# Optimization experiments

Hardware: AMD Instinct MI355X
Metric: run time of the kernel (lower is better)

## Reference

```python
import jax, jax.numpy as jnp
import numpy as np

N_NODES = 100000
N_EDGES = 1600000
F_IN, HIDDEN, N_CLASS = 256, 64, 2


def _gcn_conv(x, W, b, src, dst, norm, n):
    # PyG GCNConv: linear (no bias) -> normalized scatter-add -> bias
    h = x @ W                                  # [N, out]
    msg = h[src] * norm[:, None]               # gather + scale, [E+N, out]
    agg = jax.ops.segment_sum(msg, dst, num_segments=n)
    return agg + b


def setup_inputs() -> dict:
    key = jax.random.key(0)
    ks = jax.random.split(key, 8)
    x = jax.random.normal(ks[0], (N_NODES, F_IN), dtype=jnp.float32)
    edge_index = jax.random.randint(ks[1], (2, N_EDGES), 0, N_NODES, dtype=jnp.int32)
    W1 = jax.random.normal(ks[2], (F_IN, HIDDEN), dtype=jnp.float32) / np.sqrt(F_IN).astype(np.float32)
    b1 = jnp.zeros((HIDDEN,), dtype=jnp.float32)
    W2 = jax.random.normal(ks[3], (HIDDEN, HIDDEN), dtype=jnp.float32) / np.sqrt(HIDDEN).astype(np.float32)
    b2 = jnp.zeros((HIDDEN,), dtype=jnp.float32)
    W3 = jax.random.normal(ks[4], (HIDDEN, N_CLASS), dtype=jnp.float32) / np.sqrt(HIDDEN).astype(np.float32)
    b3 = jnp.zeros((N_CLASS,), dtype=jnp.float32)
    return {"x": x, "edge_index": edge_index, "W1": W1, "b1": b1, "W2": W2, "b2": b2, "W3": W3, "b3": b3}


def reference(x, edge_index, W1, b1, W2, b2, W3, b3):
    n = x.shape[0]
    # add self-loops (GCNConv default)
    loops = jnp.arange(n, dtype=edge_index.dtype)
    src = jnp.concatenate([edge_index[0], loops])
    dst = jnp.concatenate([edge_index[1], loops])
    # symmetric normalization D^-1/2 A_hat D^-1/2
    deg = jax.ops.segment_sum(jnp.ones_like(src, dtype=x.dtype), dst, num_segments=n)
    deg_inv_sqrt = jnp.where(deg > 0, jax.lax.rsqrt(jnp.maximum(deg, 1.0)), 0.0)
    norm = deg_inv_sqrt[src] * deg_inv_sqrt[dst]
    # layer 1 + relu (dropout is identity in eval mode)
    h = jax.nn.relu(_gcn_conv(x, W1, b1, src, dst, norm, n))
    # layer 2 + relu
    h = jax.nn.relu(_gcn_conv(h, W2, b2, src, dst, norm, n))
    # output layer + log_softmax
    h = _gcn_conv(h, W3, b3, src, dst, norm, n)
    return jax.nn.log_softmax(h, axis=1)
```

## Files before the change

kernel.cpp:

```cpp
#include <hip/hip_runtime.h>
#include <math.h>

#define F_IN 256
#define HID  64
#define BSH  8
#define BSPAN 256
#define CHUNK 16384
#define NBK_MAX 512

typedef __bf16   bf16x8 __attribute__((ext_vector_type(8)));
typedef float    floatx4 __attribute__((ext_vector_type(4)));
typedef _Float16 half8 __attribute__((ext_vector_type(8)));

__global__ __launch_bounds__(256) void k_hist(const int* __restrict__ dst,
                                              int* __restrict__ cntT,
                                              int E, int NCH, int NBK) {
    __shared__ int hist[NBK_MAX];
    int t = threadIdx.x, c = blockIdx.x;
    hist[t] = 0; hist[t + 256] = 0;
    __syncthreads();
    int base = c * CHUNK;
#pragma unroll 4
    for (int j = 0; j < CHUNK / 256; j++) {
        int e = base + j * 256 + t;
        if (e < E) atomicAdd(&hist[dst[e] >> BSH], 1);
    }
    __syncthreads();
    for (int b = t; b < NBK; b += 256) cntT[b * NCH + c] = hist[b];
}

__global__ __launch_bounds__(256) void k_scanA(const int* __restrict__ cntT,
                                               int* __restrict__ off,
                                               int* __restrict__ partials, int S) {
    __shared__ int sh[256];
    int tid = threadIdx.x;
    int base = blockIdx.x * 1024 + tid * 4;
    int v[4];
    int s = 0;
#pragma unroll
    for (int j = 0; j < 4; j++) {
        int idx = base + j;
        v[j] = (idx < S) ? cntT[idx] : 0;
        s += v[j];
    }
    sh[tid] = s;
    __syncthreads();
    int mysum = s;
    for (int o = 1; o < 256; o <<= 1) {
        int tv = (tid >= o) ? sh[tid - o] : 0;
        __syncthreads();
        sh[tid] += tv;
        __syncthreads();
    }
    int pref = sh[tid] - mysum;
#pragma unroll
    for (int j = 0; j < 4; j++) {
        int idx = base + j;
        if (idx < S) off[idx] = pref;
        pref += v[j];
    }
    if (tid == 255) partials[blockIdx.x] = sh[255];
}

__global__ void k_scanB(int* __restrict__ partials, int* __restrict__ off,
                        int nblk, int S) {
    if (blockIdx.x == 0 && threadIdx.x == 0) {
        int run = 0;
        for (int b = 0; b < nblk; b++) { int t = partials[b]; partials[b] = run; run += t; }
        off[S] = run;
    }
}

__global__ void k_scanC(int* __restrict__ off, const int* __restrict__ partials, int S) {
    int i = blockIdx.x * blockDim.x + threadIdx.x;
    if (i < S) off[i] += partials[i >> 10];
}

__global__ __launch_bounds__(256) void k_sortwrite(const int* __restrict__ src,
                                                   const int* __restrict__ dst,
                                                   const int* __restrict__ off,
                                                   int* __restrict__ ebuf,
                                                   int E, int NCH, int NBK) {
    __shared__ int cur[NBK_MAX];
    int t = threadIdx.x, c = blockIdx.x;
    for (int b = t; b < NBK; b += 256) cur[b] = off[b * NCH + c];
    __syncthreads();
    int base = c * CHUNK;
#pragma unroll 4
    for (int j = 0; j < CHUNK / 256; j++) {
        int e = base + j * 256 + t;
        if (e < E) {
            int s = src[e];
            int d = dst[e];
            int pos = atomicAdd(&cur[d >> BSH], 1);
            ebuf[pos] = (s << BSH) | (d & (BSPAN - 1));
        }
    }
}

__global__ __launch_bounds__(256) void k_bucket_csr(const int* __restrict__ off,
                                                    const int* __restrict__ ebuf,
                                                    int* __restrict__ rp,
                                                    float* __restrict__ dinv,
                                                    int* __restrict__ esrc,
                                                    int N, int NCH, int NBK) {
    __shared__ int cnt[BSPAN];
    __shared__ int sh[BSPAN];
    int b = blockIdx.x, t = threadIdx.x;
    int base = off[b * NCH];
    int end  = off[(b + 1) * NCH];

    cnt[t] = 0;
    __syncthreads();
    for (int i = base + t; i < end; i += 256) atomicAdd(&cnt[ebuf[i] & (BSPAN - 1)], 1);
    __syncthreads();

    int c = cnt[t];
    sh[t] = c;
    __syncthreads();
    for (int o = 1; o < 256; o <<= 1) {
        int tv = (t >= o) ? sh[t - o] : 0;
        __syncthreads();
        sh[t] += tv;
        __syncthreads();
    }
    int excl = sh[t] - c;

    int node = (b << BSH) + t;
    if (node < N) {
        rp[node] = base + excl;
        dinv[node] = rsqrtf((float)(1 + c));
    }
    if (b == NBK - 1 && t == 0) rp[N] = end;
    __syncthreads();

    cnt[t] = base + excl;
    __syncthreads();
    for (int i = base + t; i < end; i += 256) {
        int v = ebuf[i];
        int p = atomicAdd(&cnt[v & (BSPAN - 1)], 1);
        esrc[p] = v >> BSH;
    }
}

__global__ __launch_bounds__(256) void k_prepw(const float* __restrict__ W1,
                                               __bf16* __restrict__ f1h, __bf16* __restrict__ f1l,
                                               const float* __restrict__ W2,
                                               __bf16* __restrict__ f2h, __bf16* __restrict__ f2l) {
    int t = threadIdx.x + blockIdx.x * blockDim.x;
    for (int idx = t; idx < 16384; idx += 2048) {
        int j = idx & 7, lane = (idx >> 3) & 63, ch2 = (idx >> 9) & 7, c = idx >> 12;
        int k = ch2 * 32 + (lane >> 4) * 8 + j, col = c * 16 + (lane & 15);
        float w = W1[k * 64 + col];
        __bf16 h = (__bf16)w;
        f1h[idx] = h; f1l[idx] = (__bf16)(w - (float)h);
    }
    for (int idx = t; idx < 4096; idx += 2048) {
        int j = idx & 7, lane = (idx >> 3) & 63, ch2 = (idx >> 9) & 1, c = idx >> 10;
        int k = ch2 * 32 + (lane >> 4) * 8 + j, col = c * 16 + (lane & 15);
        float w = W2[k * 64 + col];
        __bf16 h = (__bf16)w;
        f2h[idx] = h; f2l[idx] = (__bf16)(w - (float)h);
    }
}

__global__ __launch_bounds__(256) void k_gemm1(const float* __restrict__ A,
                                               const __bf16* __restrict__ BfH,
                                               const __bf16* __restrict__ BfL,
                                               const float* __restrict__ dinv,
                                               _Float16* __restrict__ C, int nrows) {
    constexpr int K = 256, KC = 64, NCHK = 4, NCH32 = 8;
    __shared__ float As[2][64 * KC];

    const int t = threadIdx.x;
    const int wave = t >> 6, lane = t & 63;
    const int m = lane & 15, q = lane >> 4;
    const int row0 = blockIdx.x * 64;

    const int s_sub = lane >> 4;
    const int s_seg = lane & 15;

    auto stage = [&](int ch, int buf) {
#pragma unroll
        for (int j = 0; j < 4; j++) {
            int lr = wave * 16 + j * 4 + s_sub;
            int gr = row0 + lr; if (gr > nrows - 1) gr = nrows - 1;
            int gs = (s_seg - lr) & 15;
            const float* g = A + (size_t)gr * K + ch * KC + gs * 4;
            float* l = &As[buf][(size_t)lr * KC + s_seg * 4];
            __builtin_amdgcn_global_load_lds(
                (const __attribute__((address_space(1))) void*)g,
                (__attribute__((address_space(3))) void*)l, 16, 0, 0);
        }
    };

    floatx4 acc[4] = {{0.f, 0.f, 0.f, 0.f}, {0.f, 0.f, 0.f, 0.f},
                      {0.f, 0.f, 0.f, 0.f}, {0.f, 0.f, 0.f, 0.f}};

    stage(0, 0);
    __syncthreads();

    for (int ch = 0; ch < NCHK; ch++) {
        if (ch + 1 < NCHK) stage(ch + 1, (ch + 1) & 1);

        const float* arow = &As[ch & 1][(size_t)(wave * 16 + m) * KC];
#pragma unroll
        for (int jj = 0; jj < 2; jj++) {
            int ch2 = ch * 2 + jj;
            int s0 = jj * 8 + q * 2;
            float4 v0 = *(const float4*)(arow + (((s0 + m) & 15) * 4));
            float4 v1 = *(const float4*)(arow + (((s0 + 1 + m) & 15) * 4));
            float af[8] = {v0.x, v0.y, v0.z, v0.w, v1.x, v1.y, v1.z, v1.w};
            bf16x8 ah, al;
#pragma unroll
            for (int j = 0; j < 8; j++) {
                __bf16 h = (__bf16)af[j];
                ah[j] = h;
                al[j] = (__bf16)(af[j] - (float)h);
            }
#pragma unroll
            for (int c = 0; c < 4; c++) {
                const bf16x8 bh = *(const bf16x8*)(BfH + ((size_t)(c * NCH32 + ch2) * 64 + lane) * 8);
                const bf16x8 bl = *(const bf16x8*)(BfL + ((size_t)(c * NCH32 + ch2) * 64 + lane) * 8);
                acc[c] = __builtin_amdgcn_mfma_f32_16x16x32_bf16(ah, bh, acc[c], 0, 0, 0);
                acc[c] = __builtin_amdgcn_mfma_f32_16x16x32_bf16(al, bh, acc[c], 0, 0, 0);
                acc[c] = __builtin_amdgcn_mfma_f32_16x16x32_bf16(ah, bl, acc[c], 0, 0, 0);
            }
        }
        __syncthreads();
    }

#pragma unroll
    for (int i = 0; i < 4; i++) {
        int r = row0 + wave * 16 + q * 4 + i;
        if (r < nrows) {
            float di = dinv[r];
#pragma unroll
            for (int c = 0; c < 4; c++)
                C[(size_t)r * 64 + c * 16 + m] = (_Float16)(acc[c][i] * di);
        }
    }
}

__global__ __launch_bounds__(256) void k_gemm2(const _Float16* __restrict__ A,
                                               const __bf16* __restrict__ BfH,
                                               const __bf16* __restrict__ BfL,
                                               const float* __restrict__ dinv,
                                               _Float16* __restrict__ C, int nrows) {
    __shared__ _Float16 As[64 * 64];
    const int t = threadIdx.x;
    const int wave = t >> 6, lane = t & 63;
    const int m = lane & 15, q = lane >> 4;
    const int row0 = blockIdx.x * 64;

#pragma unroll
    for (int j = 0; j < 2; j++) {
        int lr = j * 32 + wave * 8 + (lane >> 3);
        int p  = lane & 7;
        int gr = row0 + lr; if (gr > nrows - 1) gr = nrows - 1;
        int gs = (p - lr) & 7;
        const _Float16* g = A + (size_t)gr * 64 + gs * 8;
        _Float16* l = &As[(size_t)lr * 64 + p * 8];
        __builtin_amdgcn_global_load_lds(
            (const __attribute__((address_space(1))) void*)g,
            (__attribute__((address_space(3))) void*)l, 16, 0, 0);
    }
    __syncthreads();

    floatx4 acc[4] = {{0.f, 0.f, 0.f, 0.f}, {0.f, 0.f, 0.f, 0.f},
                      {0.f, 0.f, 0.f, 0.f}, {0.f, 0.f, 0.f, 0.f}};

    const _Float16* arow = &As[(size_t)(wave * 16 + m) * 64];
#pragma unroll
    for (int jj = 0; jj < 2; jj++) {
        int s0 = jj * 4 + q;
        half8 v = *(const half8*)(arow + (((s0 + m) & 7) * 8));
        bf16x8 ah, al;
#pragma unroll
        for (int j = 0; j < 8; j++) {
            float f = (float)v[j];
            __bf16 h = (__bf16)f;
            ah[j] = h;
            al[j] = (__bf16)(f - (float)h);
        }
#pragma unroll
        for (int c = 0; c < 4; c++) {
            const bf16x8 bh = *(const bf16x8*)(BfH + ((size_t)(c * 2 + jj) * 64 + lane) * 8);
            const bf16x8 bl = *(const bf16x8*)(BfL + ((size_t)(c * 2 + jj) * 64 + lane) * 8);
            acc[c] = __builtin_amdgcn_mfma_f32_16x16x32_bf16(ah, bh, acc[c], 0, 0, 0);
            acc[c] = __builtin_amdgcn_mfma_f32_16x16x32_bf16(al, bh, acc[c], 0, 0, 0);
            acc[c] = __builtin_amdgcn_mfma_f32_16x16x32_bf16(ah, bl, acc[c], 0, 0, 0);
        }
    }

#pragma unroll
    for (int i = 0; i < 4; i++) {
        int r = row0 + wave * 16 + q * 4 + i;
        if (r < nrows) {
            float di = dinv[r];
#pragma unroll
            for (int c = 0; c < 4; c++)
                C[(size_t)r * 64 + c * 16 + m] = (_Float16)(acc[c][i] * di);
        }
    }
}

template <int MODE>
__global__ __launch_bounds__(256) void k_agg64(const _Float16* __restrict__ hs,
                                               const float* __restrict__ dinv,
                                               const int* __restrict__ rp,
                                               const int* __restrict__ esrc,
                                               const float* __restrict__ bias,
                                               const float* __restrict__ W3,
                                               void* __restrict__ out, int n) {
    int lane = threadIdx.x & 63;
    int nid = blockIdx.x * 4 + (threadIdx.x >> 6);
    if (nid >= n) return;
    nid = __builtin_amdgcn_readfirstlane(nid);

    float dii = dinv[nid];
    int e0 = rp[nid];
    int e1 = rp[nid + 1];

    float a0 = (float)hs[(size_t)nid * 64 + lane];
    float a1 = 0.f, a2 = 0.f, a3 = 0.f, a4 = 0.f, a5 = 0.f, a6 = 0.f, a7 = 0.f;

    for (int e = e0; e < e1; e += 8) {
        int last = e1 - 1;
        int i0 = esrc[e];
        int i1 = esrc[min(e + 1, last)];
        int i2 = esrc[min(e + 2, last)];
        int i3 = esrc[min(e + 3, last)];
        int i4 = esrc[min(e + 4, last)];
        int i5 = esrc[min(e + 5, last)];
        int i6 = esrc[min(e + 6, last)];
        int i7 = esrc[min(e + 7, last)];
        float v0 = (float)hs[(size_t)i0 * 64 + lane];
        float v1 = (float)hs[(size_t)i1 * 64 + lane];
        float v2 = (float)hs[(size_t)i2 * 64 + lane];
        float v3 = (float)hs[(size_t)i3 * 64 + lane];
        float v4 = (float)hs[(size_t)i4 * 64 + lane];
        float v5 = (float)hs[(size_t)i5 * 64 + lane];
        float v6 = (float)hs[(size_t)i6 * 64 + lane];
        float v7 = (float)hs[(size_t)i7 * 64 + lane];
        a0 += v0;
        a1 += (e + 1 <= last) ? v1 : 0.f;
        a2 += (e + 2 <= last) ? v2 : 0.f;
        a3 += (e + 3 <= last) ? v3 : 0.f;
        a4 += (e + 4 <= last) ? v4 : 0.f;
        a5 += (e + 5 <= last) ? v5 : 0.f;
        a6 += (e + 6 <= last) ? v6 : 0.f;
        a7 += (e + 7 <= last) ? v7 : 0.f;
    }

    float acc = ((a0 + a1) + (a2 + a3)) + ((a4 + a5) + (a6 + a7));
    acc = acc * dii + bias[lane];
    acc = fmaxf(acc, 0.f);

    if (MODE == 0) {
        ((_Float16*)out)[(size_t)nid * 64 + lane] = (_Float16)acc;
    } else {
        float2 w3 = ((const float2*)W3)[lane];
        float p0 = acc * w3.x;
        float p1 = acc * w3.y;
#pragma unroll
        for (int o = 32; o > 0; o >>= 1) {
            p0 += __shfl_xor(p0, o, 64);
            p1 += __shfl_xor(p1, o, 64);
        }
        if (lane == 0) ((float2*)out)[nid] = make_float2(p0 * dii, p1 * dii);
    }
}

__global__ __launch_bounds__(256) void k_final(const float2* __restrict__ h3s,
                                               const float* __restrict__ dinv,
                                               const int* __restrict__ rp,
                                               const int* __restrict__ esrc,
                                               const float* __restrict__ b3,
                                               float* __restrict__ out, int n) {
    int i = blockIdx.x * blockDim.x + threadIdx.x;
    if (i >= n) return;
    float dii = dinv[i];
    float2 h = h3s[i];
    float ax = h.x, ay = h.y;
    float bx = 0.f, by = 0.f, cx = 0.f, cy = 0.f, dx = 0.f, dy = 0.f;
    int e0 = rp[i], e1 = rp[i + 1];
    for (int e = e0; e < e1; e += 4) {
        int last = e1 - 1;
        int s0 = esrc[e];
        int s1 = esrc[min(e + 1, last)];
        int s2 = esrc[min(e + 2, last)];
        int s3 = esrc[min(e + 3, last)];
        float2 v0 = h3s[s0];
        float2 v1 = h3s[s1];
        float2 v2 = h3s[s2];
        float2 v3 = h3s[s3];
        ax += v0.x; ay += v0.y;
        bx += (e + 1 <= last) ? v1.x : 0.f; by += (e + 1 <= last) ? v1.y : 0.f;
        cx += (e + 2 <= last) ? v2.x : 0.f; cy += (e + 2 <= last) ? v2.y : 0.f;
        dx += (e + 3 <= last) ? v3.x : 0.f; dy += (e + 3 <= last) ? v3.y : 0.f;
    }
    float l0 = ((ax + bx) + (cx + dx)) * dii + b3[0];
    float l1 = ((ay + by) + (cy + dy)) * dii + b3[1];
    float m = fmaxf(l0, l1);
    float lse = m + logf(expf(l0 - m) + expf(l1 - m));
    ((float2*)out)[i] = make_float2(l0 - lse, l1 - lse);
}

extern "C" void kernel_launch(void* const* d_in, const int* in_sizes, int n_in,
                              void* d_out, int out_size, void* d_ws, size_t ws_size,
                              hipStream_t stream) {
    const float* x   = (const float*)d_in[0];
    const int*   ei  = (const int*)d_in[1];
    const float* W1  = (const float*)d_in[2];
    const float* b1  = (const float*)d_in[3];
    const float* W2  = (const float*)d_in[4];
    const float* b2  = (const float*)d_in[5];
    const float* W3  = (const float*)d_in[6];
    const float* b3  = (const float*)d_in[7];
    float* out = (float*)d_out;

    const int N = in_sizes[0] / F_IN;
    const int E = in_sizes[1] / 2;
    const int* src = ei;
    const int* dst = ei + E;

    const int NBK = (N + BSPAN - 1) / BSPAN;
    const int NCH = (E + CHUNK - 1) / CHUNK;
    const int S   = NBK * NCH;

    char* p = (char*)d_ws;
    auto alloc = [&](size_t bytes) -> void* {
        void* r = (void*)p;
        p += (bytes + 255) & ~(size_t)255;
        return r;
    };
    int*      cntT     = (int*)alloc((size_t)S * 4);
    int*      off      = (int*)alloc((size_t)(S + 1) * 4);
    int*      partials = (int*)alloc(4096);
    int*      ebuf     = (int*)alloc((size_t)E * 4);
    int*      esrc     = (int*)alloc((size_t)E * 4);
    int*      rp       = (int*)alloc((size_t)(N + 1) * 4);
    float*    dinv     = (float*)alloc((size_t)N * 4);
    _Float16* bufA     = (_Float16*)alloc((size_t)N * HID * 2);
    _Float16* bufB     = (_Float16*)alloc((size_t)N * HID * 2);
    float*    h3       = (float*)alloc((size_t)N * 2 * 4);
    __bf16*   f1h      = (__bf16*)alloc(16384 * 2);
    __bf16*   f1l      = (__bf16*)alloc(16384 * 2);
    __bf16*   f2h      = (__bf16*)alloc(4096 * 2);
    __bf16*   f2l      = (__bf16*)alloc(4096 * 2);

    const int T = 256;
    int scanBlocks = (S + 1023) / 1024;

    k_prepw<<<8, T, 0, stream>>>(W1, f1h, f1l, W2, f2h, f2l);

    k_hist<<<NCH, T, 0, stream>>>(dst, cntT, E, NCH, NBK);
    k_scanA<<<scanBlocks, T, 0, stream>>>(cntT, off, partials, S);
    k_scanB<<<1, 64, 0, stream>>>(partials, off, scanBlocks, S);
    k_scanC<<<(S + T - 1) / T, T, 0, stream>>>(off, partials, S);
    k_sortwrite<<<NCH, T, 0, stream>>>(src, dst, off, ebuf, E, NCH, NBK);
    k_bucket_csr<<<NBK, T, 0, stream>>>(off, ebuf, rp, dinv, esrc, N, NCH, NBK);

    int gemmBlocks = (N + 63) / 64;
    k_gemm1<<<gemmBlocks, T, 0, stream>>>(x, f1h, f1l, dinv, bufA, N);
    k_agg64<0><<<(N + 3) / 4, T, 0, stream>>>(bufA, dinv, rp, esrc, b1, nullptr, bufB, N);

    k_gemm2<<<gemmBlocks, T, 0, stream>>>(bufB, f2h, f2l, dinv, bufA, N);
    k_agg64<1><<<(N + 3) / 4, T, 0, stream>>>(bufA, dinv, rp, esrc, b2, W3, h3, N);

    k_final<<<(N + T - 1) / T, T, 0, stream>>>((const float2*)h3, dinv, rp, esrc, b3, out, N);
}
```

Measured before the change: 404.4 us.

## Fuse layer-1 aggregation with layer-2 GEMM, widen gathers, wave-per-node final

Merges the first-layer neighbor aggregation and the second-layer GEMM into one kernel. Each block aggregates 64 nodes into fp32 shared memory with a swizzled layout, then runs the split-bf16 MFMA on that tile. This drops the fp16 round trip through global memory and one launch. The gather loops are unrolled to 16 independent loads for more memory-level parallelism. The final 2-class aggregation now uses one wave per node with lanes over edges and a shuffle reduction. The risks are lower occupancy in the fused kernel, because each wave handles 16 nodes serially with 16 accumulators, and an underused wave in the final kernel, since nodes average about 17 edges.

```diff
diff --git a/kernel.cpp b/kernel.cpp
--- a/kernel.cpp
+++ b/kernel.cpp
@@ -242,77 +242,95 @@
     }
 }
 
-__global__ __launch_bounds__(256) void k_gemm2(const _Float16* __restrict__ A,
-                                               const __bf16* __restrict__ BfH,
-                                               const __bf16* __restrict__ BfL,
-                                               const float* __restrict__ dinv,
-                                               _Float16* __restrict__ C, int nrows) {
-    __shared__ _Float16 As[64 * 64];
+__global__ __launch_bounds__(256) void k_aggemm(const _Float16* __restrict__ hs,
+                                                const float* __restrict__ dinv,
+                                                const int* __restrict__ rp,
+                                                const int* __restrict__ esrc,
+                                                const float* __restrict__ bias,
+                                                const __bf16* __restrict__ BfH,
+                                                const __bf16* __restrict__ BfL,
+                                                _Float16* __restrict__ C, int n) {
+    __shared__ float As[64 * 64];
     const int t = threadIdx.x;
     const int wave = t >> 6, lane = t & 63;
     const int m = lane & 15, q = lane >> 4;
-    const int row0 = blockIdx.x * 64;
-
-#pragma unroll
-    for (int j = 0; j < 2; j++) {
-        int lr = j * 32 + wave * 8 + (lane >> 3);
-        int p  = lane & 7;
-        int gr = row0 + lr; if (gr > nrows - 1) gr = nrows - 1;
-        int gs = (p - lr) & 7;
-        const _Float16* g = A + (size_t)gr * 64 + gs * 8;
-        _Float16* l = &As[(size_t)lr * 64 + p * 8];
-        __builtin_amdgcn_global_load_lds(
-            (const __attribute__((address_space(1))) void*)g,
-            (__attribute__((address_space(3))) void*)l, 16, 0, 0);
-    }
-    __syncthreads();
-
-    floatx4 acc[4] = {{0.f, 0.f, 0.f, 0.f}, {0.f, 0.f, 0.f, 0.f},
-                      {0.f, 0.f, 0.f, 0.f}, {0.f, 0.f, 0.f, 0.f}};
-
-    const _Float16* arow = &As[(size_t)(wave * 16 + m) * 64];
+    const int n0 = blockIdx.x * 64;
+    const int seg = lane >> 2, off = lane & 3;
+    const float bl = bias[lane];
+
+    for (int i = 0; i < 16; i++) {
+        int lr = wave * 16 + i;
+        int nid = n0 + lr;
+        int nn = min(nid, n - 1);
+        float dii = dinv[nn];
+        int e0 = rp[nn], e1 = rp[nn + 1];
+
+        float a[16];
+        a[0] = (float)hs[(size_t)nn * 64 + lane];
+#pragma unroll
+        for (int k2 = 1; k2 < 16; k2++) a[k2] = 0.f;
+
+        for (int e = e0; e < e1; e += 16) {
+            int last = e1 - 1;
+#pragma unroll
+            for (int k2 = 0; k2 < 16; k2++) {
+                int idx = esrc[min(e + k2, last)];
+                float v = (float)hs[(size_t)idx * 64 + lane];
+                a[k2] += (e + k2 <= last) ? v : 0.f;
+            }
+        }
+        float s = (((a[0] + a[1]) + (a[2] + a[3])) + ((a[4] + a[5]) + (a[6] + a[7])))
+                + (((a[8] + a[9]) + (a[10] + a[11])) + ((a[12] + a[13]) + (a[14] + a[15])));
+        float acc = fmaxf(s * dii + bl, 0.f);
+        As[lr * 64 + (((seg + lr) & 15) << 2) + off] = (nid < n) ? acc : 0.f;
+    }
+    __syncthreads();
+
+    floatx4 acc4[4] = {{0.f, 0.f, 0.f, 0.f}, {0.f, 0.f, 0.f, 0.f},
+                       {0.f, 0.f, 0.f, 0.f}, {0.f, 0.f, 0.f, 0.f}};
+    const float* arow = &As[(size_t)(wave * 16 + m) * 64];
 #pragma unroll
     for (int jj = 0; jj < 2; jj++) {
-        int s0 = jj * 4 + q;
-        half8 v = *(const half8*)(arow + (((s0 + m) & 7) * 8));
+        int s0 = jj * 8 + q * 2;
+        float4 v0 = *(const float4*)(arow + (((s0 + m) & 15) * 4));
+        float4 v1 = *(const float4*)(arow + (((s0 + 1 + m) & 15) * 4));
+        float af[8] = {v0.x, v0.y, v0.z, v0.w, v1.x, v1.y, v1.z, v1.w};
         bf16x8 ah, al;
 #pragma unroll
         for (int j = 0; j < 8; j++) {
-            float f = (float)v[j];
-            __bf16 h = (__bf16)f;
+            __bf16 h = (__bf16)af[j];
             ah[j] = h;
-            al[j] = (__bf16)(f - (float)h);
+            al[j] = (__bf16)(af[j] - (float)h);
         }
 #pragma unroll
         for (int c = 0; c < 4; c++) {
             const bf16x8 bh = *(const bf16x8*)(BfH + ((size_t)(c * 2 + jj) * 64 + lane) * 8);
-            const bf16x8 bl = *(const bf16x8*)(BfL + ((size_t)(c * 2 + jj) * 64 + lane) * 8);
-            acc[c] = __builtin_amdgcn_mfma_f32_16x16x32_bf16(ah, bh, acc[c], 0, 0, 0);
-            acc[c] = __builtin_amdgcn_mfma_f32_16x16x32_bf16(al, bh, acc[c], 0, 0, 0);
-            acc[c] = __builtin_amdgcn_mfma_f32_16x16x32_bf16(ah, bl, acc[c], 0, 0, 0);
+            const bf16x8 bb = *(const bf16x8*)(BfL + ((size_t)(c * 2 + jj) * 64 + lane) * 8);
+            acc4[c] = __builtin_amdgcn_mfma_f32_16x16x32_bf16(ah, bh, acc4[c], 0, 0, 0);
+            acc4[c] = __builtin_amdgcn_mfma_f32_16x16x32_bf16(al, bh, acc4[c], 0, 0, 0);
+            acc4[c] = __builtin_amdgcn_mfma_f32_16x16x32_bf16(ah, bb, acc4[c], 0, 0, 0);
         }
     }
 
 #pragma unroll
     for (int i = 0; i < 4; i++) {
-        int r = row0 + wave * 16 + q * 4 + i;
-        if (r < nrows) {
+        int r = n0 + wave * 16 + q * 4 + i;
+        if (r < n) {
             float di = dinv[r];
 #pragma unroll
             for (int c = 0; c < 4; c++)
-                C[(size_t)r * 64 + c * 16 + m] = (_Float16)(acc[c][i] * di);
-        }
-    }
-}
-
-template <int MODE>
-__global__ __launch_bounds__(256) void k_agg64(const _Float16* __restrict__ hs,
-                                               const float* __restrict__ dinv,
-                                               const int* __restrict__ rp,
-                                               const int* __restrict__ esrc,
-                                               const float* __restrict__ bias,
-                                               const float* __restrict__ W3,
-                                               void* __restrict__ out, int n) {
+                C[(size_t)r * 64 + c * 16 + m] = (_Float16)(acc4[c][i] * di);
+        }
+    }
+}
+
+__global__ __launch_bounds__(256) void k_agg_w3(const _Float16* __restrict__ hs,
+                                                const float* __restrict__ dinv,
+                                                const int* __restrict__ rp,
+                                                const int* __restrict__ esrc,
+                                                const float* __restrict__ bias,
+                                                const float* __restrict__ W3,
+                                                float2* __restrict__ h3, int n) {
     int lane = threadIdx.x & 63;
     int nid = blockIdx.x * 4 + (threadIdx.x >> 6);
     if (nid >= n) return;
@@ -322,54 +340,33 @@
     int e0 = rp[nid];
     int e1 = rp[nid + 1];
 
-    float a0 = (float)hs[(size_t)nid * 64 + lane];
-    float a1 = 0.f, a2 = 0.f, a3 = 0.f, a4 = 0.f, a5 = 0.f, a6 = 0.f, a7 = 0.f;
-
-    for (int e = e0; e < e1; e += 8) {
+    float a[16];
+    a[0] = (float)hs[(size_t)nid * 64 + lane];
+#pragma unroll
+    for (int k2 = 1; k2 < 16; k2++) a[k2] = 0.f;
+
+    for (int e = e0; e < e1; e += 16) {
         int last = e1 - 1;
-        int i0 = esrc[e];
-        int i1 = esrc[min(e + 1, last)];
-        int i2 = esrc[min(e + 2, last)];
-        int i3 = esrc[min(e + 3, last)];
-        int i4 = esrc[min(e + 4, last)];
-        int i5 = esrc[min(e + 5, last)];
-        int i6 = esrc[min(e + 6, last)];
-        int i7 = esrc[min(e + 7, last)];
-        float v0 = (float)hs[(size_t)i0 * 64 + lane];
-        float v1 = (float)hs[(size_t)i1 * 64 + lane];
-        float v2 = (float)hs[(size_t)i2 * 64 + lane];
-        float v3 = (float)hs[(size_t)i3 * 64 + lane];
-        float v4 = (float)hs[(size_t)i4 * 64 + lane];
-        float v5 = (float)hs[(size_t)i5 * 64 + lane];
-        float v6 = (float)hs[(size_t)i6 * 64 + lane];
-        float v7 = (float)hs[(size_t)i7 * 64 + lane];
-        a0 += v0;
-        a1 += (e + 1 <= last) ? v1 : 0.f;
-        a2 += (e + 2 <= last) ? v2 : 0.f;
-        a3 += (e + 3 <= last) ? v3 : 0.f;
-        a4 += (e + 4 <= last) ? v4 : 0.f;
-        a5 += (e + 5 <= last) ? v5 : 0.f;
-        a6 += (e + 6 <= last) ? v6 : 0.f;
-        a7 += (e + 7 <= last) ? v7 : 0.f;
-    }
-
-    float acc = ((a0 + a1) + (a2 + a3)) + ((a4 + a5) + (a6 + a7));
-    acc = acc * dii + bias[lane];
-    acc = fmaxf(acc, 0.f);
-
-    if (MODE == 0) {
-        ((_Float16*)out)[(size_t)nid * 64 + lane] = (_Float16)acc;
-    } else {
-        float2 w3 = ((const float2*)W3)[lane];
-        float p0 = acc * w3.x;
-        float p1 = acc * w3.y;
-#pragma unroll
-        for (int o = 32; o > 0; o >>= 1) {
-            p0 += __shfl_xor(p0, o, 64);
-            p1 += __shfl_xor(p1, o, 64);
-        }
-        if (lane == 0) ((float2*)out)[nid] = make_float2(p0 * dii, p1 * dii);
-    }
+#pragma unroll
+        for (int k2 = 0; k2 < 16; k2++) {
+            int idx = esrc[min(e + k2, last)];
+            float v = (float)hs[(size_t)idx * 64 + lane];
+            a[k2] += (e + k2 <= last) ? v : 0.f;
+        }
+    }
+    float s = (((a[0] + a[1]) + (a[2] + a[3])) + ((a[4] + a[5]) + (a[6] + a[7])))
+            + (((a[8] + a[9]) + (a[10] + a[11])) + ((a[12] + a[13]) + (a[14] + a[15])));
+    float acc = fmaxf(s * dii + bias[lane], 0.f);
+
+    float2 w3 = ((const float2*)W3)[lane];
+    float p0 = acc * w3.x;
+    float p1 = acc * w3.y;
+#pragma unroll
+    for (int o = 32; o > 0; o >>= 1) {
+        p0 += __shfl_xor(p0, o, 64);
+        p1 += __shfl_xor(p1, o, 64);
+    }
+    if (lane == 0) h3[nid] = make_float2(p0 * dii, p1 * dii);
 }
 
 __global__ __launch_bounds__(256) void k_final(const float2* __restrict__ h3s,
@@ -378,33 +375,35 @@
                                                const int* __restrict__ esrc,
                                                const float* __restrict__ b3,
                                                float* __restrict__ out, int n) {
-    int i = blockIdx.x * blockDim.x + threadIdx.x;
-    if (i >= n) return;
-    float dii = dinv[i];
-    float2 h = h3s[i];
-    float ax = h.x, ay = h.y;
-    float bx = 0.f, by = 0.f, cx = 0.f, cy = 0.f, dx = 0.f, dy = 0.f;
-    int e0 = rp[i], e1 = rp[i + 1];
-    for (int e = e0; e < e1; e += 4) {
-        int last = e1 - 1;
-        int s0 = esrc[e];
-        int s1 = esrc[min(e + 1, last)];
-        int s2 = esrc[min(e + 2, last)];
-        int s3 = esrc[min(e + 3, last)];
-        float2 v0 = h3s[s0];
-        float2 v1 = h3s[s1];
-        float2 v2 = h3s[s2];
-        float2 v3 = h3s[s3];
-        ax += v0.x; ay += v0.y;
-        bx += (e + 1 <= last) ? v1.x : 0.f; by += (e + 1 <= last) ? v1.y : 0.f;
-        cx += (e + 2 <= last) ? v2.x : 0.f; cy += (e + 2 <= last) ? v2.y : 0.f;
-        dx += (e + 3 <= last) ? v3.x : 0.f; dy += (e + 3 <= last) ? v3.y : 0.f;
-    }
-    float l0 = ((ax + bx) + (cx + dx)) * dii + b3[0];
-    float l1 = ((ay + by) + (cy + dy)) * dii + b3[1];
-    float m = fmaxf(l0, l1);
-    float lse = m + logf(expf(l0 - m) + expf(l1 - m));
-    ((float2*)out)[i] = make_float2(l0 - lse, l1 - lse);
+    int lane = threadIdx.x & 63;
+    int nid = blockIdx.x * 4 + (threadIdx.x >> 6);
+    if (nid >= n) return;
+    nid = __builtin_amdgcn_readfirstlane(nid);
+
+    int e0 = rp[nid], e1 = rp[nid + 1];
+    float ax = 0.f, ay = 0.f;
+    for (int e = e0; e < e1; e += 64) {
+        int idx = e + lane;
+        int s = esrc[min(idx, e1 - 1)];
+        float2 v = h3s[s];
+        bool valid = idx < e1;
+        ax += valid ? v.x : 0.f;
+        ay += valid ? v.y : 0.f;
+    }
+#pragma unroll
+    for (int o = 32; o > 0; o >>= 1) {
+        ax += __shfl_xor(ax, o, 64);
+        ay += __shfl_xor(ay, o, 64);
+    }
+    if (lane == 0) {
+        float dii = dinv[nid];
+        float2 h = h3s[nid];
+        float l0 = (h.x + ax) * dii + b3[0];
+        float l1 = (h.y + ay) * dii + b3[1];
+        float m = fmaxf(l0, l1);
+        float lse = m + logf(expf(l0 - m) + expf(l1 - m));
+        ((float2*)out)[nid] = make_float2(l0 - lse, l1 - lse);
+    }
 }
 
 extern "C" void kernel_launch(void* const* d_in, const int* in_sizes, int n_in,
@@ -464,10 +463,10 @@
 
     int gemmBlocks = (N + 63) / 64;
     k_gemm1<<<gemmBlocks, T, 0, stream>>>(x, f1h, f1l, dinv, bufA, N);
-    k_agg64<0><<<(N + 3) / 4, T, 0, stream>>>(bufA, dinv, rp, esrc, b1, nullptr, bufB, N);
-
-    k_gemm2<<<gemmBlocks, T, 0, stream>>>(bufB, f2h, f2l, dinv, bufA, N);
-    k_agg64<1><<<(N + 3) / 4, T, 0, stream>>>(bufA, dinv, rp, esrc, b2, W3, h3, N);
-
-    k_final<<<(N + T - 1) / T, T, 0, stream>>>((const float2*)h3, dinv, rp, esrc, b3, out, N);
-}
+
+    k_aggemm<<<gemmBlocks, T, 0, stream>>>(bufA, dinv, rp, esrc, b1, f2h, f2l, bufB, N);
+
+    k_agg_w3<<<(N + 3) / 4, T, 0, stream>>>(bufB, dinv, rp, esrc, b2, W3, (float2*)h3, N);
+
+    k_final<<<(N + 3) / 4, T, 0, stream>>>((const float2*)h3, dinv, rp, esrc, b3, out, N);
+}
```

Result: slower. 475.2 us (+17.5%).
